# Optimization experiments

Hardware: AMD Instinct MI355X
Metric: run time of the kernel (lower is better)

## Reference

```python
import jax, jax.numpy as jnp
import numpy as np

N_NODES = 50000
N_EDGES = 800000
K = 15          # kernel points
P_DIM = 3
IN_DIM = 32
OUT_DIM = 64
KP_EXTENT = 0.6


def setup_inputs() -> dict:
    key = jax.random.key(0)
    k1, k2, k3, k4, k5, k6 = jax.random.split(key, 6)
    pos = jax.random.normal(k1, (N_NODES, P_DIM), dtype=jnp.float32)
    feat = jax.random.normal(k2, (N_NODES, IN_DIM), dtype=jnp.float32)
    # kernel point layout inside a ball of the given radius (load_kernels stand-in)
    kernel_points = jax.random.normal(k3, (K, P_DIM), dtype=jnp.float32) * 0.5
    kernel_points = kernel_points.at[0].set(0.0)  # fixed center point
    weights = jax.random.normal(k4, (K, IN_DIM, OUT_DIM), dtype=jnp.float32) * (1.0 / np.sqrt(IN_DIM))
    edge_src = jax.random.randint(k5, (N_EDGES,), 0, N_NODES, dtype=jnp.int32)
    edge_dst = jax.random.randint(k6, (N_EDGES,), 0, N_NODES, dtype=jnp.int32)
    return {"pos": pos, "feat": feat, "kernel_points": kernel_points,
            "weights": weights, "edge_src": edge_src, "edge_dst": edge_dst}


def reference(pos, feat, kernel_points, weights, edge_src, edge_dst):
    n_nodes = pos.shape[0]
    # per-edge relative position: src - dst  [E, p]
    y = pos[edge_src] - pos[edge_dst]
    # distance to each kernel point  [E, k]
    diff = y[:, None, :] - kernel_points[None, :, :]
    dist = jnp.sqrt(jnp.sum(diff * diff, axis=-1))
    # linear correlation influence  [E, k]
    m = jax.nn.relu(1.0 - dist / KP_EXTENT)
    # per-edge weighted features  [E, k, in]
    f = feat[edge_src]
    contrib = m[:, :, None] * f[:, None, :]
    # segment-reduce onto destination nodes  [N, k, in]
    weighted_f = jax.ops.segment_sum(contrib, edge_dst, num_segments=n_nodes)
    # per-kernel-point matmul and sum over kernel points  [N, out]
    return jnp.einsum('nki,kio->no', weighted_f, weights)
```

## Files before the change

kernel.cpp:

```cpp
#include <hip/hip_runtime.h>
#include <hip/hip_bf16.h>

#define N_NODES 50000
#define N_EDGES 800000
#define KPTS 15
#define IN_DIM 32
#define OUT_DIM 64
#define KP_EXTENT 0.6f
#define INV_EXT (1.0f / KP_EXTENT)
#define EXT2 (KP_EXTENT * KP_EXTENT)

#define CAP 131072
#define NREP 16
#define SEG_CAP (CAP / NREP)
#define CNT_STRIDE 32
#define K1_BLOCKS (N_EDGES / 256)
#define SUBB 16

#define PCNT_OFF 32768
#define LIST_OFF 262144
#define SLOT_OFF 16777216
#define SCAP_MAX 8

__global__ __launch_bounds__(256) void geom_compact(
    const float* __restrict__ pos,
    const float* __restrict__ kp,
    const int*   __restrict__ esrc,
    const int*   __restrict__ edst,
    int*         __restrict__ cnt,
    uint2*       __restrict__ lists,
    float4*      __restrict__ outz)
{
    __shared__ int s_wavecnt[KPTS][4];
    __shared__ int s_woff[KPTS][4];
    __shared__ int s_base[KPTS];

    const int tid  = threadIdx.x;
    const int wv   = tid >> 6;
    const int lane = tid & 63;
    const int rep  = blockIdx.x & (NREP - 1);

    const int e = blockIdx.x * 256 + tid;

    outz[e] = make_float4(0.0f, 0.0f, 0.0f, 0.0f);

    const int s = esrc[e];
    const int d = edst[e];

    const float yx = pos[s * 3 + 0] - pos[d * 3 + 0];
    const float yy = pos[s * 3 + 1] - pos[d * 3 + 1];
    const float yz = pos[s * 3 + 2] - pos[d * 3 + 2];

    float d2v[KPTS];
    unsigned act = 0;
    #pragma unroll
    for (int k = 0; k < KPTS; ++k) {
        const float dx = yx - kp[k * 3 + 0];
        const float dy = yy - kp[k * 3 + 1];
        const float dz = yz - kp[k * 3 + 2];
        const float d2 = dx * dx + dy * dy + dz * dz;
        d2v[k] = d2;
        if (d2 < EXT2) act |= (1u << k);
    }

    #pragma unroll
    for (int k = 0; k < KPTS; ++k) {
        const unsigned long long mask = __ballot((act >> k) & 1u);
        if (lane == 0) s_wavecnt[k][wv] = __popcll(mask);
    }
    __syncthreads();

    if (tid < KPTS) {
        int o0 = 0;
        #pragma unroll
        for (int w = 0; w < 4; ++w) {
            s_woff[tid][w] = o0;
            o0 += s_wavecnt[tid][w];
        }
        s_base[tid] = (o0 > 0)
            ? atomicAdd(&cnt[(tid * NREP + rep) * CNT_STRIDE], o0) : 0;
    }
    __syncthreads();

    const unsigned long long lt = (lane == 63) ? 0x7fffffffffffffffull
                                               : ((1ull << lane) - 1ull);
    const unsigned sd = ((unsigned)s << 16) | (unsigned)d;
    #pragma unroll
    for (int k = 0; k < KPTS; ++k) {
        const bool a = (act >> k) & 1u;
        const unsigned long long mask = __ballot(a);
        if (a) {
            const int rank = __popcll(mask & lt);
            const int idx  = s_base[k] + s_woff[k][wv] + rank;
            if (idx < SEG_CAP)
                lists[(size_t)k * CAP + (size_t)rep * SEG_CAP + idx] =
                    make_uint2(sd, __float_as_uint(d2v[k]));
        }
    }
}

__global__ __launch_bounds__(256) void pair_matmul(
    const float* __restrict__ feat,
    const float* __restrict__ W,
    const int*   __restrict__ cnt,
    const uint2* __restrict__ lists,
    float*       __restrict__ out,
    int*         __restrict__ pcnt,
    float*       __restrict__ slots,
    const int scap)
{
    const int seg  = blockIdx.x % (KPTS * NREP);
    const int sub  = blockIdx.x / (KPTS * NREP);
    const int k    = seg >> 4;
    const int rep  = seg & (NREP - 1);
    const int wv   = threadIdx.x >> 6;
    const int lane = threadIdx.x & 63;

    float w[IN_DIM];
    #pragma unroll
    for (int i = 0; i < IN_DIM; ++i)
        w[i] = W[k * (IN_DIM * OUT_DIM) + i * OUT_DIM + lane];
    #pragma unroll
    for (int i = 0; i < IN_DIM; ++i)
        asm volatile("" : "+v"(w[i]));

    int n = cnt[seg * CNT_STRIDE];
    if (n > SEG_CAP) n = SEG_CAP;
    const uint2* __restrict__ list =
        lists + (size_t)k * CAP + (size_t)rep * SEG_CAP;

    const int widx    = sub * 4 + wv;
    const int stride2 = SUBB * 4 * 2;

    for (int base = widx * 2; base < n; base += stride2) {
        if (base + 1 < n) {
            const uint4 ee = *reinterpret_cast<const uint4*>(list + base);
            const unsigned sd0 = (unsigned)__builtin_amdgcn_readfirstlane((int)ee.x);
            const unsigned sd1 = (unsigned)__builtin_amdgcn_readfirstlane((int)ee.z);
            const float m0 = 1.0f - sqrtf(fmaxf(__uint_as_float(ee.y), 0.0f)) * INV_EXT;
            const float m1 = 1.0f - sqrtf(fmaxf(__uint_as_float(ee.w), 0.0f)) * INV_EXT;

            const float* __restrict__ f0 = feat + ((sd0 >> 16) << 5);
            const float* __restrict__ f1 = feat + ((sd1 >> 16) << 5);

            float a0 = 0.0f, b0 = 0.0f, a1 = 0.0f, b1 = 0.0f;
            #pragma unroll
            for (int i = 0; i < 16; ++i) {
                a0 = fmaf(f0[i],      w[i],      a0);
                b0 = fmaf(f0[i + 16], w[i + 16], b0);
                a1 = fmaf(f1[i],      w[i],      a1);
                b1 = fmaf(f1[i + 16], w[i + 16], b1);
            }
            const float r0 = m0 * (a0 + b0);
            const float r1 = m1 * (a1 + b1);
            const int d0 = (int)(sd0 & 0xffffu);
            const int d1 = (int)(sd1 & 0xffffu);

            int t = 0;
            if (lane == 0) t = atomicAdd(pcnt + d0, 1);
            if (lane == 1) t = atomicAdd(pcnt + d1, 1);
            const int s0 = __shfl(t, 0);
            const int s1 = __shfl(t, 1);

            if (s0 < scap) slots[((size_t)d0 * scap + s0) * OUT_DIM + lane] = r0;
            else           atomicAdd(out + (size_t)d0 * OUT_DIM + lane, r0);
            if (s1 < scap) slots[((size_t)d1 * scap + s1) * OUT_DIM + lane] = r1;
            else           atomicAdd(out + (size_t)d1 * OUT_DIM + lane, r1);
        } else {
            const uint2 ent = list[base];
            const unsigned sd = (unsigned)__builtin_amdgcn_readfirstlane((int)ent.x);
            const float m = 1.0f - sqrtf(fmaxf(__uint_as_float(ent.y), 0.0f)) * INV_EXT;
            const float* __restrict__ f = feat + ((sd >> 16) << 5);

            float a = 0.0f, b = 0.0f;
            #pragma unroll
            for (int i = 0; i < 16; ++i) {
                a = fmaf(f[i],      w[i],      a);
                b = fmaf(f[i + 16], w[i + 16], b);
            }
            const float r = m * (a + b);
            const int d = (int)(sd & 0xffffu);

            int t = 0;
            if (lane == 0) t = atomicAdd(pcnt + d, 1);
            const int s0 = __shfl(t, 0);

            if (s0 < scap) slots[((size_t)d * scap + s0) * OUT_DIM + lane] = r;
            else           atomicAdd(out + (size_t)d * OUT_DIM + lane, r);
        }
    }
}

__global__ __launch_bounds__(256) void node_reduce(
    const int*   __restrict__ pcnt,
    const float* __restrict__ slots,
    float*       __restrict__ out,
    const int scap)
{
    const int wv   = threadIdx.x >> 6;
    const int lane = threadIdx.x & 63;
    const int node = blockIdx.x * 4 + wv;

    const int raw = pcnt[node];
    int deg = raw;
    if (deg > scap) deg = scap;

    const float* __restrict__ sp = slots + ((size_t)node * scap) * OUT_DIM + lane;

    float a0 = (raw > scap) ? out[(size_t)node * OUT_DIM + lane] : 0.0f;
    float a1 = 0.0f;

    int j = 0;
    for (; j + 1 < deg; j += 2) {
        a0 += sp[(size_t)j * OUT_DIM];
        a1 += sp[(size_t)(j + 1) * OUT_DIM];
    }
    if (j < deg) a1 += sp[(size_t)j * OUT_DIM];

    out[(size_t)node * OUT_DIM + lane] = a0 + a1;
}

extern "C" void kernel_launch(void* const* d_in, const int* in_sizes, int n_in,
                              void* d_out, int out_size, void* d_ws, size_t ws_size,
                              hipStream_t stream)
{
    const float* pos  = (const float*)d_in[0];
    const float* feat = (const float*)d_in[1];
    const float* kp   = (const float*)d_in[2];
    const float* W    = (const float*)d_in[3];
    const int* esrc   = (const int*)d_in[4];
    const int* edst   = (const int*)d_in[5];
    float* out        = (float*)d_out;

    int*   cnt   = (int*)d_ws;
    int*   pcnt  = (int*)((char*)d_ws + PCNT_OFF);
    uint2* lists = (uint2*)((char*)d_ws + LIST_OFF);
    float* slots = (float*)((char*)d_ws + SLOT_OFF);

    const size_t layer_bytes = (size_t)N_NODES * OUT_DIM * sizeof(float);
    int scap = 0;
    if (ws_size >= (size_t)SLOT_OFF + layer_bytes) {
        scap = (int)((ws_size - (size_t)SLOT_OFF) / layer_bytes);
        if (scap > SCAP_MAX) scap = SCAP_MAX;
    }

    hipMemsetAsync(d_ws, 0, LIST_OFF, stream);

    geom_compact<<<K1_BLOCKS, 256, 0, stream>>>(pos, kp, esrc, edst, cnt, lists,
                                                (float4*)out);
    pair_matmul<<<SUBB * KPTS * NREP, 256, 0, stream>>>(feat, W, cnt, lists, out,
                                                        pcnt, slots, scap);
    if (scap > 0)
        node_reduce<<<N_NODES / 4, 256, 0, stream>>>(pcnt, slots, out, scap);
}
```

Baseline: 140.0 us.

## Move slot allocation into geometry kernel and prefetch list entries in matmul

```diff
diff --git a/kernel.cpp b/kernel.cpp
--- a/kernel.cpp
+++ b/kernel.cpp
@@ -1,5 +1,5 @@
 #include <hip/hip_runtime.h>
-#include <hip/hip_bf16.h>
+#include <hip/hip_fp16.h>
 
 #define N_NODES 50000
 #define N_EDGES 800000
@@ -28,8 +28,10 @@
     const int*   __restrict__ esrc,
     const int*   __restrict__ edst,
     int*         __restrict__ cnt,
+    int*         __restrict__ pcnt,
     uint2*       __restrict__ lists,
-    float4*      __restrict__ outz)
+    float4*      __restrict__ outz,
+    const int scap)
 {
     __shared__ int s_wavecnt[KPTS][4];
     __shared__ int s_woff[KPTS][4];
@@ -84,7 +86,6 @@
 
     const unsigned long long lt = (lane == 63) ? 0x7fffffffffffffffull
                                                : ((1ull << lane) - 1ull);
-    const unsigned sd = ((unsigned)s << 16) | (unsigned)d;
     #pragma unroll
     for (int k = 0; k < KPTS; ++k) {
         const bool a = (act >> k) & 1u;
@@ -92,9 +93,19 @@
         if (a) {
             const int rank = __popcll(mask & lt);
             const int idx  = s_base[k] + s_woff[k][wv] + rank;
-            if (idx < SEG_CAP)
+            if (idx < SEG_CAP) {
+                const float mk = 1.0f - sqrtf(d2v[k]) * INV_EXT;
+                __half hm = __float2half(mk);
+                const unsigned mh = *reinterpret_cast<unsigned short*>(&hm);
+
+                const int t = atomicAdd(pcnt + d, 1);
+                const unsigned ey = (t < scap)
+                    ? (unsigned)((d * scap + t) * OUT_DIM)
+                    : (0x80000000u | (unsigned)d);
+
                 lists[(size_t)k * CAP + (size_t)rep * SEG_CAP + idx] =
-                    make_uint2(sd, __float_as_uint(d2v[k]));
+                    make_uint2(((unsigned)s << 16) | mh, ey);
+            }
         }
     }
 }
@@ -105,9 +116,7 @@
     const int*   __restrict__ cnt,
     const uint2* __restrict__ lists,
     float*       __restrict__ out,
-    int*         __restrict__ pcnt,
-    float*       __restrict__ slots,
-    const int scap)
+    float*       __restrict__ slots)
 {
     const int seg  = blockIdx.x % (KPTS * NREP);
     const int sub  = blockIdx.x / (KPTS * NREP);
@@ -132,17 +141,30 @@
     const int widx    = sub * 4 + wv;
     const int stride2 = SUBB * 4 * 2;
 
-    for (int base = widx * 2; base < n; base += stride2) {
-        if (base + 1 < n) {
-            const uint4 ee = *reinterpret_cast<const uint4*>(list + base);
-            const unsigned sd0 = (unsigned)__builtin_amdgcn_readfirstlane((int)ee.x);
-            const unsigned sd1 = (unsigned)__builtin_amdgcn_readfirstlane((int)ee.z);
-            const float m0 = 1.0f - sqrtf(fmaxf(__uint_as_float(ee.y), 0.0f)) * INV_EXT;
-            const float m1 = 1.0f - sqrtf(fmaxf(__uint_as_float(ee.w), 0.0f)) * INV_EXT;
-
-            const float* __restrict__ f0 = feat + ((sd0 >> 16) << 5);
-            const float* __restrict__ f1 = feat + ((sd1 >> 16) << 5);
-
+    int base = widx * 2;
+    if (base >= n) return;
+
+    uint4 ee = *reinterpret_cast<const uint4*>(list + base);
+
+    for (; base < n; base += stride2) {
+        const int nb = base + stride2;
+        const uint4 en = *reinterpret_cast<const uint4*>(list + (nb < n ? nb : 0));
+
+        const unsigned ex0 = (unsigned)__builtin_amdgcn_readfirstlane((int)ee.x);
+        const unsigned ey0 = (unsigned)__builtin_amdgcn_readfirstlane((int)ee.y);
+        const bool two = (base + 1 < n);
+        const unsigned ex1 = (unsigned)__builtin_amdgcn_readfirstlane((int)ee.z);
+        const unsigned ey1 = (unsigned)__builtin_amdgcn_readfirstlane((int)ee.w);
+
+        __half h0; *reinterpret_cast<unsigned short*>(&h0) = (unsigned short)(ex0 & 0xffffu);
+        __half h1; *reinterpret_cast<unsigned short*>(&h1) = (unsigned short)(ex1 & 0xffffu);
+        const float m0 = __half2float(h0);
+        const float m1 = __half2float(h1);
+
+        const float* __restrict__ f0 = feat + ((ex0 >> 16) << 5);
+        const float* __restrict__ f1 = feat + ((ex1 >> 16) << 5);
+
+        if (two) {
             float a0 = 0.0f, b0 = 0.0f, a1 = 0.0f, b1 = 0.0f;
             #pragma unroll
             for (int i = 0; i < 16; ++i) {
@@ -153,41 +175,24 @@
             }
             const float r0 = m0 * (a0 + b0);
             const float r1 = m1 * (a1 + b1);
-            const int d0 = (int)(sd0 & 0xffffu);
-            const int d1 = (int)(sd1 & 0xffffu);
-
-            int t = 0;
-            if (lane == 0) t = atomicAdd(pcnt + d0, 1);
-            if (lane == 1) t = atomicAdd(pcnt + d1, 1);
-            const int s0 = __shfl(t, 0);
-            const int s1 = __shfl(t, 1);
-
-            if (s0 < scap) slots[((size_t)d0 * scap + s0) * OUT_DIM + lane] = r0;
-            else           atomicAdd(out + (size_t)d0 * OUT_DIM + lane, r0);
-            if (s1 < scap) slots[((size_t)d1 * scap + s1) * OUT_DIM + lane] = r1;
-            else           atomicAdd(out + (size_t)d1 * OUT_DIM + lane, r1);
+
+            if (!(ey0 & 0x80000000u)) slots[(size_t)ey0 + lane] = r0;
+            else atomicAdd(out + (size_t)(ey0 & 0xffffu) * OUT_DIM + lane, r0);
+            if (!(ey1 & 0x80000000u)) slots[(size_t)ey1 + lane] = r1;
+            else atomicAdd(out + (size_t)(ey1 & 0xffffu) * OUT_DIM + lane, r1);
         } else {
-            const uint2 ent = list[base];
-            const unsigned sd = (unsigned)__builtin_amdgcn_readfirstlane((int)ent.x);
-            const float m = 1.0f - sqrtf(fmaxf(__uint_as_float(ent.y), 0.0f)) * INV_EXT;
-            const float* __restrict__ f = feat + ((sd >> 16) << 5);
-
-            float a = 0.0f, b = 0.0f;
+            float a0 = 0.0f, b0 = 0.0f;
             #pragma unroll
             for (int i = 0; i < 16; ++i) {
-                a = fmaf(f[i],      w[i],      a);
-                b = fmaf(f[i + 16], w[i + 16], b);
+                a0 = fmaf(f0[i],      w[i],      a0);
+                b0 = fmaf(f0[i + 16], w[i + 16], b0);
             }
-            const float r = m * (a + b);
-            const int d = (int)(sd & 0xffffu);
-
-            int t = 0;
-            if (lane == 0) t = atomicAdd(pcnt + d, 1);
-            const int s0 = __shfl(t, 0);
-
-            if (s0 < scap) slots[((size_t)d * scap + s0) * OUT_DIM + lane] = r;
-            else           atomicAdd(out + (size_t)d * OUT_DIM + lane, r);
+            const float r0 = m0 * (a0 + b0);
+            if (!(ey0 & 0x80000000u)) slots[(size_t)ey0 + lane] = r0;
+            else atomicAdd(out + (size_t)(ey0 & 0xffffu) * OUT_DIM + lane, r0);
         }
+
+        ee = en;
     }
 }
 
@@ -246,10 +251,10 @@
 
     hipMemsetAsync(d_ws, 0, LIST_OFF, stream);
 
-    geom_compact<<<K1_BLOCKS, 256, 0, stream>>>(pos, kp, esrc, edst, cnt, lists,
-                                                (float4*)out);
-    pair_matmul<<<SUBB * KPTS * NREP, 256, 0, stream>>>(feat, W, cnt, lists, out,
-                                                        pcnt, slots, scap);
+    geom_compact<<<K1_BLOCKS, 256, 0, stream>>>(pos, kp, esrc, edst, cnt, pcnt,
+                                                lists, (float4*)out, scap);
+    pair_matmul<<<SUBB * KPTS * NREP, 256, 0, stream>>>(feat, W, cnt, lists,
+                                                        out, slots);
     if (scap > 0)
         node_reduce<<<N_NODES / 4, 256, 0, stream>>>(pcnt, slots, out, scap);
 }
```

Result: faster. 134.2 us (-4.2%).
